# Performance work log

Hardware: AMD Instinct MI355X
Metric: run time of the kernel (lower is better)

The kernel has to match this reference:

```python
import jax, jax.numpy as jnp
import numpy as np

N_NODES = 50000
N_EDGES = 640000
IN_F, HID_F, OUT_F = 128, 256, 128


def setup_inputs() -> dict:
    key = jax.random.key(0)
    k_x, k_e, k_w1, k_w2 = jax.random.split(key, 4)
    x = jax.random.normal(k_x, (N_NODES, IN_F), dtype=jnp.float32)
    edge_index = jax.random.randint(k_e, (2, N_EDGES), 0, N_NODES, dtype=jnp.int32)
    # Glorot-ish init for the two GCNConv linear layers
    W1 = jax.random.normal(k_w1, (IN_F, HID_F), dtype=jnp.float32) / np.sqrt(IN_F)
    b1 = jnp.zeros((HID_F,), dtype=jnp.float32)
    W2 = jax.random.normal(k_w2, (HID_F, OUT_F), dtype=jnp.float32) / np.sqrt(HID_F)
    b2 = jnp.zeros((OUT_F,), dtype=jnp.float32)
    return {"x": x, "edge_index": edge_index, "W1": W1, "b1": b1, "W2": W2, "b2": b2}


def gcn_conv(x, W, b, src, dst, n):
    """GCNConv with add_self_loops=True, normalize=True (symmetric D^-1/2 A D^-1/2)."""
    h = x @ W  # [n, out]
    loop = jnp.arange(n, dtype=src.dtype)
    s = jnp.concatenate([src, loop])  # [E+n]
    d = jnp.concatenate([dst, loop])
    deg = jax.ops.segment_sum(jnp.ones_like(s, dtype=h.dtype), d, num_segments=n)
    dinv = jnp.where(deg > 0, jax.lax.rsqrt(deg), 0.0)
    norm = dinv[s] * dinv[d]  # [E+n]
    out = jax.ops.segment_sum(h[s] * norm[:, None], d, num_segments=n)  # scatter-add
    return out + b


def reference(x, edge_index, W1, b1, W2, b2):
    src, dst = edge_index[0], edge_index[1]
    n = x.shape[0]
    h = jax.nn.relu(gcn_conv(x, W1, b1, src, dst, n))
    # dropout is identity in eval/deterministic mode
    return gcn_conv(h, W2, b2, src, dst, n)
```

## Files before the change

kernel.cpp:

```cpp
#include <hip/hip_runtime.h>
#include <math.h>


constexpr int NN = 50000;
constexpr int NE = 640000;
constexpr int F_IN = 128;
constexpr int F_HID = 256;
constexpr int F_OUT = 128;
constexpr int CAP = 64;

typedef __attribute__((ext_vector_type(8))) short bf16x8;
typedef __attribute__((ext_vector_type(4))) float f32x4;
typedef __attribute__((ext_vector_type(8))) unsigned short u16x8;

__device__ inline unsigned short f2bf(float v) {
    unsigned int u = __float_as_uint(v);
    return (unsigned short)((u + 0x7fff + ((u >> 16) & 1)) >> 16);
}
__device__ inline float bf2f(unsigned short h) {
    return __uint_as_float(((unsigned int)h) << 16);
}

template <int K, int N>
__device__ inline void wpack_one(const float* __restrict__ W,
                                 unsigned short* __restrict__ hi,
                                 unsigned short* __restrict__ lo, int t) {
    constexpr int NT = N / 16;
    int lane = t & 63, nt = (t >> 6) % NT, kt = (t >> 6) / NT;
    int col = nt * 16 + (lane & 15), kg = lane >> 4;
    unsigned short hb[8], lb[8];
#pragma unroll
    for (int e = 0; e < 8; ++e) {
        int k = kt * 32 + kg * 8 + e;
        float v = W[(size_t)k * N + col];
        unsigned short h = f2bf(v);
        hb[e] = h;
        lb[e] = f2bf(v - bf2f(h));
    }
    *reinterpret_cast<u16x8*>(hi + (size_t)t * 8) = *reinterpret_cast<u16x8*>(hb);
    *reinterpret_cast<u16x8*>(lo + (size_t)t * 8) = *reinterpret_cast<u16x8*>(lb);
}

constexpr int G_FILL = (NE + 255) / 256;
__global__ __launch_bounds__(256) void k_fill_wpack(
    const int* __restrict__ src, const int* __restrict__ dst,
    int* __restrict__ cnt, int* __restrict__ bucket,
    const float* __restrict__ W1, unsigned short* __restrict__ W1hi,
    unsigned short* __restrict__ W1lo,
    const float* __restrict__ W2, unsigned short* __restrict__ W2hi,
    unsigned short* __restrict__ W2lo) {
    if (blockIdx.x < G_FILL) {
        int e = blockIdx.x * 256 + threadIdx.x;
        if (e >= NE) return;
        int d = dst[e];
        int slot = atomicAdd(&cnt[d], 1);
        bucket[(size_t)d * CAP + slot] = src[e];
    } else {
        constexpr int T1 = (F_IN / 32) * (F_HID / 16) * 64;
        constexpr int T2 = (F_HID / 32) * (F_OUT / 16) * 64;
        int t = (blockIdx.x - G_FILL) * 256 + threadIdx.x;
        if (t < T1) {
            wpack_one<F_IN, F_HID>(W1, W1hi, W1lo, t);
        } else if (t < T1 + T2) {
            wpack_one<F_HID, F_OUT>(W2, W2hi, W2lo, t - T1);
        }
    }
}

constexpr int G_CONV = NN * 16 / 256;
__global__ __launch_bounds__(256) void k_conv_dinv(
    const int* __restrict__ cnt, const float* __restrict__ x,
    unsigned short* __restrict__ xs, float* __restrict__ dinv) {
    int gid = blockIdx.x * 256 + threadIdx.x;
    int node = gid >> 4, c = gid & 15;
    if (node >= NN) return;
    float di = rsqrtf((float)(cnt[node] + 1));
    if (c == 0) dinv[node] = di;
    float4 v0 = reinterpret_cast<const float4*>(x)[(size_t)node * 32 + c * 2];
    float4 v1 = reinterpret_cast<const float4*>(x)[(size_t)node * 32 + c * 2 + 1];
    unsigned short o[8];
    o[0] = f2bf(di * v0.x); o[1] = f2bf(di * v0.y);
    o[2] = f2bf(di * v0.z); o[3] = f2bf(di * v0.w);
    o[4] = f2bf(di * v1.x); o[5] = f2bf(di * v1.y);
    o[6] = f2bf(di * v1.z); o[7] = f2bf(di * v1.w);
    reinterpret_cast<u16x8*>(xs)[(size_t)node * 16 + c] = *reinterpret_cast<u16x8*>(o);
}

__global__ __launch_bounds__(256) void k_mega1(
    const unsigned short* __restrict__ xs, const int* __restrict__ bucket,
    const int* __restrict__ cnt, const float* __restrict__ dinv,
    const unsigned short* __restrict__ B1hi, const unsigned short* __restrict__ B1lo,
    const float* __restrict__ bias1,
    const unsigned short* __restrict__ B2hi, const unsigned short* __restrict__ B2lo,
    unsigned short* __restrict__ H2b) {
    __shared__ unsigned short Ahi_s[16][136];
    __shared__ unsigned short Alo_s[16][136];
    __shared__ unsigned short H1_s[16][264];
    __shared__ float dinv_s[16];
    const int tid = threadIdx.x;
    const int row = tid >> 4;
    const int c = tid & 15;
    const int node = blockIdx.x * 16 + row;

    const float di = dinv[node];
    if (c == 0) dinv_s[row] = di;
    const u16x8* fb = reinterpret_cast<const u16x8*>(xs);
    float acc[8];
    {
        u16x8 v = fb[(size_t)node * 16 + c];
#pragma unroll
        for (int k = 0; k < 8; ++k) acc[k] = bf2f(v[k]);
    }
    const int* blist = bucket + (size_t)node * CAP;
    const int end = cnt[node];
    int j = 0;
    for (; j + 3 < end; j += 4) {
        int s0 = blist[j], s1 = blist[j + 1], s2 = blist[j + 2], s3 = blist[j + 3];
        u16x8 r0 = fb[(size_t)s0 * 16 + c];
        u16x8 r1 = fb[(size_t)s1 * 16 + c];
        u16x8 r2 = fb[(size_t)s2 * 16 + c];
        u16x8 r3 = fb[(size_t)s3 * 16 + c];
#pragma unroll
        for (int k = 0; k < 8; ++k)
            acc[k] += (bf2f(r0[k]) + bf2f(r1[k])) + (bf2f(r2[k]) + bf2f(r3[k]));
    }
    for (; j < end; ++j) {
        u16x8 r = fb[(size_t)blist[j] * 16 + c];
#pragma unroll
        for (int k = 0; k < 8; ++k) acc[k] += bf2f(r[k]);
    }
    {
        unsigned short hb[8], lb[8];
#pragma unroll
        for (int k = 0; k < 8; ++k) {
            float v = acc[k] * di;
            hb[k] = f2bf(v);
            lb[k] = f2bf(v - bf2f(hb[k]));
        }
        *reinterpret_cast<u16x8*>(&Ahi_s[row][c * 8]) = *reinterpret_cast<u16x8*>(hb);
        *reinterpret_cast<u16x8*>(&Alo_s[row][c * 8]) = *reinterpret_cast<u16x8*>(lb);
    }
    __syncthreads();

    const int lane = tid & 63;
    const int wv = tid >> 6;
    const int r16 = lane & 15;
    const int kg = lane >> 4;
    const int ccol = lane & 15;
    const int crow0 = (lane >> 4) * 4;
    {
        f32x4 acc2[4];
#pragma unroll
        for (int ct = 0; ct < 4; ++ct) acc2[ct] = (f32x4){0.f, 0.f, 0.f, 0.f};
        const unsigned short* pb_hi = B1hi + (size_t)lane * 8;
        const unsigned short* pb_lo = B1lo + (size_t)lane * 8;
#pragma unroll
        for (int kt = 0; kt < 4; ++kt) {
            bf16x8 ah = *reinterpret_cast<const bf16x8*>(&Ahi_s[r16][kt * 32 + kg * 8]);
            bf16x8 al = *reinterpret_cast<const bf16x8*>(&Alo_s[r16][kt * 32 + kg * 8]);
#pragma unroll
            for (int ct = 0; ct < 4; ++ct) {
                const int nt = wv * 4 + ct;
                bf16x8 bh = *reinterpret_cast<const bf16x8*>(pb_hi + (size_t)(kt * 16 + nt) * 512);
                bf16x8 bl = *reinterpret_cast<const bf16x8*>(pb_lo + (size_t)(kt * 16 + nt) * 512);
                acc2[ct] = __builtin_amdgcn_mfma_f32_16x16x32_bf16(ah, bh, acc2[ct], 0, 0, 0);
                acc2[ct] = __builtin_amdgcn_mfma_f32_16x16x32_bf16(ah, bl, acc2[ct], 0, 0, 0);
                acc2[ct] = __builtin_amdgcn_mfma_f32_16x16x32_bf16(al, bh, acc2[ct], 0, 0, 0);
            }
        }
#pragma unroll
        for (int ct = 0; ct < 4; ++ct) {
            int col = (wv * 4 + ct) * 16 + ccol;
            float bv = bias1[col];
#pragma unroll
            for (int i = 0; i < 4; ++i) {
                float v = fmaxf(acc2[ct][i] + bv, 0.f);
                H1_s[crow0 + i][col] = f2bf(v);
            }
        }
    }
    __syncthreads();

    {
        f32x4 acc3[2];
        acc3[0] = (f32x4){0.f, 0.f, 0.f, 0.f};
        acc3[1] = (f32x4){0.f, 0.f, 0.f, 0.f};
        const unsigned short* pb_hi = B2hi + (size_t)lane * 8;
        const unsigned short* pb_lo = B2lo + (size_t)lane * 8;
#pragma unroll
        for (int kt = 0; kt < 8; ++kt) {
            bf16x8 a = *reinterpret_cast<const bf16x8*>(&H1_s[r16][kt * 32 + kg * 8]);
#pragma unroll
            for (int ct = 0; ct < 2; ++ct) {
                const int nt = wv * 2 + ct;
                bf16x8 bh = *reinterpret_cast<const bf16x8*>(pb_hi + (size_t)(kt * 8 + nt) * 512);
                bf16x8 bl = *reinterpret_cast<const bf16x8*>(pb_lo + (size_t)(kt * 8 + nt) * 512);
                acc3[ct] = __builtin_amdgcn_mfma_f32_16x16x32_bf16(a, bh, acc3[ct], 0, 0, 0);
                acc3[ct] = __builtin_amdgcn_mfma_f32_16x16x32_bf16(a, bl, acc3[ct], 0, 0, 0);
            }
        }
#pragma unroll
        for (int ct = 0; ct < 2; ++ct) {
            int col = (wv * 2 + ct) * 16 + ccol;
#pragma unroll
            for (int i = 0; i < 4; ++i) {
                float v = acc3[ct][i] * dinv_s[crow0 + i];
                H2b[(size_t)(blockIdx.x * 16 + crow0 + i) * F_OUT + col] = f2bf(v);
            }
        }
    }
}

__global__ __launch_bounds__(256) void k_gather_bf(
    const unsigned short* __restrict__ feat, const int* __restrict__ bucket,
    const int* __restrict__ cnt, const float* __restrict__ dinv,
    const float* __restrict__ bias, float* __restrict__ out_f) {
    int node = blockIdx.x * 16 + (threadIdx.x >> 4);
    int c = threadIdx.x & 15;
    if (node >= NN) return;
    const u16x8* fb = reinterpret_cast<const u16x8*>(feat);
    float acc[8];
    {
        u16x8 v = fb[(size_t)node * 16 + c];
#pragma unroll
        for (int k = 0; k < 8; ++k) acc[k] = bf2f(v[k]);
    }
    const int* blist = bucket + (size_t)node * CAP;
    const int end = cnt[node];
    int j = 0;
    for (; j + 3 < end; j += 4) {
        int s0 = blist[j], s1 = blist[j + 1], s2 = blist[j + 2], s3 = blist[j + 3];
        u16x8 r0 = fb[(size_t)s0 * 16 + c];
        u16x8 r1 = fb[(size_t)s1 * 16 + c];
        u16x8 r2 = fb[(size_t)s2 * 16 + c];
        u16x8 r3 = fb[(size_t)s3 * 16 + c];
#pragma unroll
        for (int k = 0; k < 8; ++k)
            acc[k] += (bf2f(r0[k]) + bf2f(r1[k])) + (bf2f(r2[k]) + bf2f(r3[k]));
    }
    for (; j < end; ++j) {
        u16x8 r = fb[(size_t)blist[j] * 16 + c];
#pragma unroll
        for (int k = 0; k < 8; ++k) acc[k] += bf2f(r[k]);
    }
    float di = dinv[node];
    float4 o0, o1;
    const float4* b4 = reinterpret_cast<const float4*>(bias);
    float4 b0 = b4[c * 2], b1 = b4[c * 2 + 1];
    o0.x = acc[0] * di + b0.x; o0.y = acc[1] * di + b0.y;
    o0.z = acc[2] * di + b0.z; o0.w = acc[3] * di + b0.w;
    o1.x = acc[4] * di + b1.x; o1.y = acc[5] * di + b1.y;
    o1.z = acc[6] * di + b1.z; o1.w = acc[7] * di + b1.w;
    float4* o4 = reinterpret_cast<float4*>(out_f);
    o4[(size_t)node * 32 + c * 2] = o0;
    o4[(size_t)node * 32 + c * 2 + 1] = o1;
}

extern "C" void kernel_launch(void* const* d_in, const int* in_sizes, int n_in,
                              void* d_out, int out_size, void* d_ws, size_t ws_size,
                              hipStream_t stream) {
    const float* x  = (const float*)d_in[0];
    const int*   ei = (const int*)d_in[1];
    const float* W1 = (const float*)d_in[2];
    const float* b1 = (const float*)d_in[3];
    const float* W2 = (const float*)d_in[4];
    const float* b2 = (const float*)d_in[5];
    float* out = (float*)d_out;

    const int* src = ei;
    const int* dst = ei + NE;

    char* ws = (char*)d_ws;
    int*   cnt     = (int*)ws;
    float* dinv    = (float*)(ws + 262144);
    unsigned short* W1hi = (unsigned short*)(ws + 524288);
    unsigned short* W1lo = (unsigned short*)(ws + 589824);
    unsigned short* W2hi = (unsigned short*)(ws + 655360);
    unsigned short* W2lo = (unsigned short*)(ws + 720896);
    int*   bucket  = (int*)(ws + 1048576);
    unsigned short* xs   = (unsigned short*)(ws + 14680064);
    unsigned short* H2b  = (unsigned short*)(ws + 28311552);

    constexpr int BT = 256;
    const int gG = NN / 16;

    hipMemsetAsync(cnt, 0, NN * sizeof(int), stream);
    k_fill_wpack<<<G_FILL + 32, BT, 0, stream>>>(
        src, dst, cnt, bucket, W1, W1hi, W1lo, W2, W2hi, W2lo);
    k_conv_dinv<<<G_CONV, BT, 0, stream>>>(cnt, x, xs, dinv);

    k_mega1<<<gG, BT, 0, stream>>>(xs, bucket, cnt, dinv,
                                   W1hi, W1lo, b1, W2hi, W2lo, H2b);
    k_gather_bf<<<gG, BT, 0, stream>>>(H2b, bucket, cnt, dinv, b2, out);
}
```

Measured before the change: 131.9 us.

## Sort nodes by in-degree so gather blocks process balanced neighbor counts

Adds a degree histogram to the dinv kernel and a counting-sort scatter kernel that builds a permutation of nodes grouped by in-degree. Both aggregation kernels then process nodes in permuted order, so the 16 rows of a block have similar neighbor counts and less lane divergence in the gather loops. The cost is an extra kernel launch, atomics on a small histogram, indirect node indexing, and scattered output writes that lose row contiguity.

Measured after the change: 481.7 us. 265% more time.

```diff
diff --git a/kernel.cpp b/kernel.cpp
--- a/kernel.cpp
+++ b/kernel.cpp
@@ -70,12 +70,17 @@
 constexpr int G_CONV = NN * 16 / 256;
 __global__ __launch_bounds__(256) void k_conv_dinv(
     const int* __restrict__ cnt, const float* __restrict__ x,
-    unsigned short* __restrict__ xs, float* __restrict__ dinv) {
+    unsigned short* __restrict__ xs, float* __restrict__ dinv,
+    int* __restrict__ hist) {
     int gid = blockIdx.x * 256 + threadIdx.x;
     int node = gid >> 4, c = gid & 15;
     if (node >= NN) return;
-    float di = rsqrtf((float)(cnt[node] + 1));
-    if (c == 0) dinv[node] = di;
+    int deg = cnt[node];
+    float di = rsqrtf((float)(deg + 1));
+    if (c == 0) {
+        dinv[node] = di;
+        atomicAdd(&hist[min(deg, 63)], 1);
+    }
     float4 v0 = reinterpret_cast<const float4*>(x)[(size_t)node * 32 + c * 2];
     float4 v1 = reinterpret_cast<const float4*>(x)[(size_t)node * 32 + c * 2 + 1];
     unsigned short o[8];
@@ -86,9 +91,32 @@
     reinterpret_cast<u16x8*>(xs)[(size_t)node * 16 + c] = *reinterpret_cast<u16x8*>(o);
 }
 
+constexpr int G_SC = (NN + 255) / 256;
+__global__ __launch_bounds__(256) void k_scatter(
+    const int* __restrict__ cnt, const int* __restrict__ hist,
+    int* __restrict__ cur, int* __restrict__ perm) {
+    __shared__ int boff[64];
+    if (threadIdx.x < 64) {
+        int s = 0;
+#pragma unroll 1
+        for (int i = 0; i < 64; ++i) {
+            if (i == threadIdx.x) break;
+            s += hist[i];
+        }
+        boff[threadIdx.x] = s;
+    }
+    __syncthreads();
+    int v = blockIdx.x * 256 + threadIdx.x;
+    if (v >= NN) return;
+    int deg = min(cnt[v], 63);
+    int pos = boff[deg] + atomicAdd(&cur[deg], 1);
+    perm[pos] = v;
+}
+
 __global__ __launch_bounds__(256) void k_mega1(
     const unsigned short* __restrict__ xs, const int* __restrict__ bucket,
     const int* __restrict__ cnt, const float* __restrict__ dinv,
+    const int* __restrict__ perm,
     const unsigned short* __restrict__ B1hi, const unsigned short* __restrict__ B1lo,
     const float* __restrict__ bias1,
     const unsigned short* __restrict__ B2hi, const unsigned short* __restrict__ B2lo,
@@ -97,13 +125,14 @@
     __shared__ unsigned short Alo_s[16][136];
     __shared__ unsigned short H1_s[16][264];
     __shared__ float dinv_s[16];
+    __shared__ int node_s[16];
     const int tid = threadIdx.x;
     const int row = tid >> 4;
     const int c = tid & 15;
-    const int node = blockIdx.x * 16 + row;
+    const int node = perm[blockIdx.x * 16 + row];
 
     const float di = dinv[node];
-    if (c == 0) dinv_s[row] = di;
+    if (c == 0) { dinv_s[row] = di; node_s[row] = node; }
     const u16x8* fb = reinterpret_cast<const u16x8*>(xs);
     float acc[8];
     {
@@ -205,7 +234,7 @@
 #pragma unroll
             for (int i = 0; i < 4; ++i) {
                 float v = acc3[ct][i] * dinv_s[crow0 + i];
-                H2b[(size_t)(blockIdx.x * 16 + crow0 + i) * F_OUT + col] = f2bf(v);
+                H2b[(size_t)node_s[crow0 + i] * F_OUT + col] = f2bf(v);
             }
         }
     }
@@ -214,10 +243,10 @@
 __global__ __launch_bounds__(256) void k_gather_bf(
     const unsigned short* __restrict__ feat, const int* __restrict__ bucket,
     const int* __restrict__ cnt, const float* __restrict__ dinv,
+    const int* __restrict__ perm,
     const float* __restrict__ bias, float* __restrict__ out_f) {
-    int node = blockIdx.x * 16 + (threadIdx.x >> 4);
+    int node = perm[blockIdx.x * 16 + (threadIdx.x >> 4)];
     int c = threadIdx.x & 15;
-    if (node >= NN) return;
     const u16x8* fb = reinterpret_cast<const u16x8*>(feat);
     float acc[8];
     {
@@ -271,12 +300,15 @@
     const int* dst = ei + NE;
 
     char* ws = (char*)d_ws;
-    int*   cnt     = (int*)ws;
-    float* dinv    = (float*)(ws + 262144);
-    unsigned short* W1hi = (unsigned short*)(ws + 524288);
-    unsigned short* W1lo = (unsigned short*)(ws + 589824);
-    unsigned short* W2hi = (unsigned short*)(ws + 655360);
-    unsigned short* W2lo = (unsigned short*)(ws + 720896);
+    int*   cnt  = (int*)ws;
+    int*   hist = (int*)(ws + 200704);
+    int*   cur  = (int*)(ws + 200960);
+    float* dinv = (float*)(ws + 262144);
+    int*   perm = (int*)(ws + 524288);
+    unsigned short* W1hi = (unsigned short*)(ws + 786432);
+    unsigned short* W1lo = (unsigned short*)(ws + 851968);
+    unsigned short* W2hi = (unsigned short*)(ws + 917504);
+    unsigned short* W2lo = (unsigned short*)(ws + 983040);
     int*   bucket  = (int*)(ws + 1048576);
     unsigned short* xs   = (unsigned short*)(ws + 14680064);
     unsigned short* H2b  = (unsigned short*)(ws + 28311552);
@@ -284,12 +316,13 @@
     constexpr int BT = 256;
     const int gG = NN / 16;
 
-    hipMemsetAsync(cnt, 0, NN * sizeof(int), stream);
+    hipMemsetAsync(cnt, 0, 201216, stream);
     k_fill_wpack<<<G_FILL + 32, BT, 0, stream>>>(
         src, dst, cnt, bucket, W1, W1hi, W1lo, W2, W2hi, W2lo);
-    k_conv_dinv<<<G_CONV, BT, 0, stream>>>(cnt, x, xs, dinv);
-
-    k_mega1<<<gG, BT, 0, stream>>>(xs, bucket, cnt, dinv,
+    k_conv_dinv<<<G_CONV, BT, 0, stream>>>(cnt, x, xs, dinv, hist);
+    k_scatter<<<G_SC, BT, 0, stream>>>(cnt, hist, cur, perm);
+
+    k_mega1<<<gG, BT, 0, stream>>>(xs, bucket, cnt, dinv, perm,
                                    W1hi, W1lo, b1, W2hi, W2lo, H2b);
-    k_gather_bf<<<gG, BT, 0, stream>>>(H2b, bucket, cnt, dinv, b2, out);
-}
+    k_gather_bf<<<gG, BT, 0, stream>>>(H2b, bucket, cnt, dinv, perm, b2, out);
+}
```
